# Kernel tuning notes

Measured on AMD Instinct MI355X. Metric: run time of the kernel, lower is better.

## Reference

```python
import jax, jax.numpy as jnp
import numpy as np

SEQ = 2048
D = 2048          # d_model
H = 16            # n_heads
DH = D // H       # dim_per_head = 128 (= pe_rotary_dims, full-head RoPE)
DFF = 4 * D
BACKGROUND_LEN = 1024
STYLE_VECS_LEN = 64


def setup_inputs() -> dict:
    key = jax.random.key(0)
    ks = jax.random.split(key, 12)
    s = 0.02
    f32 = jnp.float32
    return {
        "x": jax.random.normal(ks[0], (SEQ, D), f32),
        "attn_bias": jnp.zeros((SEQ, SEQ), f32),
        "ln_scale": jnp.ones((D,), f32),
        "ln_offset": jnp.zeros((D,), f32),
        "Wq": (jax.random.normal(ks[1], (D, D), f32) * s),
        "Wk": (jax.random.normal(ks[2], (D, D), f32) * s),
        "Wv": (jax.random.normal(ks[3], (D, D), f32) * s),
        "Wo": (jax.random.normal(ks[4], (D, D), f32) * s),
        "W1": (jax.random.normal(ks[5], (D, DFF), f32) * s),
        "b1": jnp.zeros((DFF,), f32),
        "W2": (jax.random.normal(ks[6], (DFF, D), f32) * s),
        "b2": jnp.zeros((D,), f32),
    }


def _layernorm(x, scale, offset):
    mean = jnp.mean(x, axis=-1, keepdims=True)
    var = jnp.var(x, axis=-1, keepdims=True)
    return scale * jax.lax.rsqrt(var + 1e-5) * (x - mean) + offset


def _rotate_every_two(x):
    # x: (T, H, d) -> interleaved (-x2, x1)
    x1 = x[:, :, ::2]
    x2 = x[:, :, 1::2]
    return jnp.stack((-x2, x1), axis=-1).reshape(x.shape)


def _apply_rope(q, k):
    rd = q.shape[-1]
    inv_freq = 1.0 / 10000 ** (np.arange(0, rd, 2) / rd)  # (rd/2,)
    pos = jnp.arange(k.shape[0])
    sinusoid = pos[:, None] * inv_freq[None, :]           # (T, rd/2)
    # repeat 'b n -> b (n j)', j=2  ==  elementwise repeat along last axis
    sin = jnp.repeat(jnp.sin(sinusoid), 2, axis=-1)[:, None, :]  # (T,1,rd)
    cos = jnp.repeat(jnp.cos(sinusoid), 2, axis=-1)[:, None, :]
    q = q * cos + _rotate_every_two(q) * sin
    k = k * cos + _rotate_every_two(k) * sin
    return q, k


def _causal_bottleneck_bias():
    mask = np.tril(np.ones((SEQ, SEQ), np.float32))
    # DO_CAUSAL_BOTTLENECK: tokens after background+style cannot see background
    mask[BACKGROUND_LEN + STYLE_VECS_LEN:, :BACKGROUND_LEN] = 0.0
    return jnp.asarray(-1e10 * (1.0 - mask))


def reference(x, attn_bias, ln_scale, ln_offset, Wq, Wk, Wv, Wo, W1, b1, W2, b2):
    # f_psum / g_psum are identities with cores_per_replica == 1
    xn = _layernorm(x, ln_scale, ln_offset)                      # (T, D)

    q = (xn @ Wq).reshape(SEQ, H, DH)
    k = (xn @ Wk).reshape(SEQ, H, DH)
    v = (xn @ Wv).reshape(SEQ, H, DH)

    q, k = _apply_rope(q, k)  # pe_rotary_dims == dim_per_head: rotate whole head

    logits = jnp.einsum('thd,Thd->htT', q, k) / np.sqrt(DH).astype(x.dtype)
    bias = _causal_bottleneck_bias() + attn_bias                 # (T, T)
    logits = logits + bias[None, :, :]
    weights = jax.nn.softmax(logits, axis=-1)                    # (H, T, T)

    attn_vec = jnp.einsum('htT,Thd->thd', weights, v).reshape(SEQ, D)
    attn_out = attn_vec @ Wo                                     # (T, D)

    ff = jax.nn.gelu(xn @ W1 + b1) @ W2 + b2                     # (T, D)
    return attn_out + ff
```

## Files before the change

### kernel.cpp

```cpp
#include <hip/hip_runtime.h>

#define SEQ 2048
#define DMODEL 2048
#define NH 16
#define DH 128
#define DFF 8192

typedef __bf16 bf16x8 __attribute__((ext_vector_type(8)));
typedef float f32x4 __attribute__((ext_vector_type(4)));
typedef int i32x4 __attribute__((ext_vector_type(4)));

__device__ __forceinline__ float b2f(unsigned short u) {
    union { float f; unsigned int i; } v; v.i = ((unsigned int)u) << 16; return v.f;
}
__device__ __forceinline__ unsigned short f2b(float f) {
    union { float f; unsigned int i; } v; v.f = f;
    unsigned int i = v.i;
    i += 0x7fffu + ((i >> 16) & 1u);
    return (unsigned short)(i >> 16);
}
__device__ __forceinline__ bf16x8 ldfrag(const unsigned short* p) {
    return *(const bf16x8*)p;
}
__device__ __forceinline__ void async_ld16(const unsigned short* g, unsigned short* l) {
    __builtin_amdgcn_global_load_lds(
        (const __attribute__((address_space(1))) unsigned int*)g,
        (__attribute__((address_space(3))) unsigned int*)l, 16, 0, 0);
}
__device__ __forceinline__ float loadef(const void* p, long i, int isf) {
    return isf ? ((const float*)p)[i] : b2f(((const unsigned short*)p)[i]);
}
__device__ __forceinline__ void load8f(const void* p, long i, int isf, float* v) {
    if (isf) {
        i32x4 r0 = *(const i32x4*)((const float*)p + i);
        i32x4 r1 = *(const i32x4*)((const float*)p + i + 4);
        const float* f0 = (const float*)&r0;
        const float* f1 = (const float*)&r1;
#pragma unroll
        for (int j = 0; j < 4; j++) { v[j] = f0[j]; v[4 + j] = f1[j]; }
    } else {
        i32x4 raw = *(const i32x4*)((const unsigned short*)p + i);
        const unsigned short* u = (const unsigned short*)&raw;
#pragma unroll
        for (int j = 0; j < 8; j++) v[j] = b2f(u[j]);
    }
}

__global__ __launch_bounds__(256) void detect_kernel(const unsigned short* __restrict__ x,
                                                     int* __restrict__ flag)
{
    const int tid = threadIdx.x;
    int bad = 0;
#pragma unroll
    for (int i = 0; i < 16; i++) {
        unsigned short u = x[tid * 16 + i];
        int e = (u >> 7) & 0xFF;
        if (e >= 0x90) bad = 1;
    }
    unsigned long long b = __ballot(bad);
    __shared__ int r[4];
    if ((tid & 63) == 0) r[tid >> 6] = (b != 0ull);
    __syncthreads();
    if (tid == 0) *flag = (r[0] | r[1] | r[2] | r[3]) ? 1 : 0;
}

__global__ __launch_bounds__(256) void ln_kernel(
    const void* __restrict__ x,
    const void* __restrict__ sc,
    const void* __restrict__ of,
    unsigned short* __restrict__ xn,
    const int* __restrict__ fl)
{
    const int isf = *fl;
    const int row = blockIdx.x, tid = threadIdx.x;
    float v[8]; float s = 0.f, sq = 0.f;
    load8f(x, (long)row * DMODEL + tid * 8, isf, v);
#pragma unroll
    for (int i = 0; i < 8; i++) { s += v[i]; sq += v[i] * v[i]; }
#pragma unroll
    for (int off = 1; off < 64; off <<= 1) { s += __shfl_xor(s, off); sq += __shfl_xor(sq, off); }
    __shared__ float red[8];
    const int w = tid >> 6, l = tid & 63;
    if (l == 0) { red[w * 2] = s; red[w * 2 + 1] = sq; }
    __syncthreads();
    s  = red[0] + red[2] + red[4] + red[6];
    sq = red[1] + red[3] + red[5] + red[7];
    const float mean = s * (1.0f / DMODEL);
    const float var  = sq * (1.0f / DMODEL) - mean * mean;
    const float rsig = rsqrtf(var + 1e-5f);
    __align__(16) unsigned short o[8];
#pragma unroll
    for (int i = 0; i < 8; i++) {
        int c = tid * 8 + i;
        o[i] = f2b(loadef(sc, c, isf) * (v[i] - mean) * rsig + loadef(of, c, isf));
    }
    *(i32x4*)(xn + (long)row * DMODEL + tid * 8) = *(const i32x4*)o;
}

__global__ __launch_bounds__(1024) void transpose_w(
    const void* __restrict__ in, unsigned short* __restrict__ out, int R, int C,
    const int* __restrict__ fl)
{
    const int isf = *fl;
    __shared__ unsigned short tile[32][33];
    const int tx = threadIdx.x, ty = threadIdx.y;
    const int c0 = blockIdx.x * 32, r0 = blockIdx.y * 32;
    tile[ty][tx] = f2b(loadef(in, (long)(r0 + ty) * C + c0 + tx, isf));
    __syncthreads();
    out[(long)(c0 + ty) * R + r0 + tx] = tile[tx][ty];
}

__global__ __launch_bounds__(256) void rope_kernel(unsigned short* q, unsigned short* k)
{
    const int idx = blockIdx.x * 256 + threadIdx.x;
    const int i = idx & 63;
    const int h = (idx >> 6) & 15;
    const int t = idx >> 10;
    const long base = (long)t * DMODEL + h * DH + 2 * i;
    const float inv = __expf(-(float)i * (9.210340371976184f / 64.0f));
    float sn, cs;
    sincosf((float)t * inv, &sn, &cs);
    {
        float a = b2f(q[base]), b = b2f(q[base + 1]);
        q[base]     = f2b(a * cs - b * sn);
        q[base + 1] = f2b(b * cs + a * sn);
    }
    {
        float a = b2f(k[base]), b = b2f(k[base + 1]);
        k[base]     = f2b(a * cs - b * sn);
        k[base + 1] = f2b(b * cs + a * sn);
    }
}

template<int EPI>
__global__ __launch_bounds__(256) void gemm_bt(
    const unsigned short* __restrict__ A,
    const unsigned short* __restrict__ Bt,
    const void* __restrict__ bias,
    const unsigned short* __restrict__ add,
    void* __restrict__ Cout,
    int M, int N, int K, int Ks,
    const int* __restrict__ fl)
{
    const int isf = fl ? *fl : 0;
    __shared__ __align__(16) unsigned short lA[128 * 32];
    __shared__ __align__(16) unsigned short lB[128 * 32];
    const int tid = threadIdx.x;
    const int l = tid & 63, w = tid >> 6;
    const int quad = l >> 4, lq = l & 15;
    const long bm = (long)blockIdx.y * 128, bn = (long)blockIdx.x * 128;
    const int wm = (w >> 1) * 64, wn = (w & 1) * 64;
    const int kofs = (EPI == 5) ? blockIdx.z * Ks : 0;

    const int srow = w * 32 + (l >> 2);
    const int scol = (l & 3) * 8;
    const unsigned short* Ag0 = A  + (bm + srow) * (long)K + kofs + scol;
    const unsigned short* Ag1 = Ag0 + 16 * (long)K;
    const unsigned short* Bg0 = Bt + (bn + srow) * (long)K + kofs + scol;
    const unsigned short* Bg1 = Bg0 + 16 * (long)K;
    unsigned short* lAd = lA + w * 1024 + l * 8;
    unsigned short* lBd = lB + w * 1024 + l * 8;

    f32x4 acc[4][4] = {};

    for (int k0 = 0; k0 < Ks; k0 += 32) {
        async_ld16(Ag0 + k0, lAd);
        async_ld16(Ag1 + k0, lAd + 512);
        async_ld16(Bg0 + k0, lBd);
        async_ld16(Bg1 + k0, lBd + 512);
        __syncthreads();
        bf16x8 af[4], bfv[4];
#pragma unroll
        for (int i = 0; i < 4; i++) af[i]  = ldfrag(lA + (wm + i * 16 + lq) * 32 + quad * 8);
#pragma unroll
        for (int j = 0; j < 4; j++) bfv[j] = ldfrag(lB + (wn + j * 16 + lq) * 32 + quad * 8);
#pragma unroll
        for (int i = 0; i < 4; i++)
#pragma unroll
            for (int j = 0; j < 4; j++)
                acc[i][j] = __builtin_amdgcn_mfma_f32_16x16x32_bf16(af[i], bfv[j], acc[i][j], 0, 0, 0);
        __syncthreads();
    }

#pragma unroll
    for (int i = 0; i < 4; i++)
#pragma unroll
        for (int j = 0; j < 4; j++)
#pragma unroll
            for (int r = 0; r < 4; r++) {
                const long t = bm + wm + i * 16 + quad * 4 + r;
                const long n = bn + wn + j * 16 + lq;
                float v = acc[i][j][r];
                if constexpr (EPI == 5) {
                    ((float*)Cout)[(long)blockIdx.z * M * N + t * N + n] = v;
                } else if constexpr (EPI == 4) {
                    unsigned short* base = (unsigned short*)Cout;
                    if (n < 4096)
                        base[(n >> 11) * (long)(SEQ * DMODEL) + t * DMODEL + (n & 2047)] = f2b(v);
                    else {
                        const long np = n - 4096;
                        base[2L * SEQ * DMODEL + (np >> 7) * (long)(DH * SEQ) + (np & 127) * (long)SEQ + t] = f2b(v);
                    }
                } else if constexpr (EPI == 3) {
                    v += loadef(bias, n, isf) + b2f(add[t * (long)N + n]);
                    if (isf) ((float*)Cout)[t * (long)N + n] = v;
                    else     ((unsigned short*)Cout)[t * (long)N + n] = f2b(v);
                } else {
                    if constexpr (EPI == 2) {
                        v += loadef(bias, n, isf);
                        v = 0.5f * v * (1.0f + tanhf(0.7978845608028654f * (v + 0.044715f * v * v * v)));
                    }
                    ((unsigned short*)Cout)[t * (long)N + n] = f2b(v);
                }
            }
}

__global__ __launch_bounds__(256) void reduce_out(
    const float* __restrict__ P, int nsplit,
    const unsigned short* __restrict__ aout,
    const void* __restrict__ b2,
    void* __restrict__ out,
    const int* __restrict__ fl)
{
    const int isf = *fl;
    const long i = ((long)blockIdx.x * 256 + threadIdx.x) * 4;
    f32x4 s = *(const f32x4*)(P + i);
    for (int z = 1; z < nsplit; z++) s += *(const f32x4*)(P + (long)z * SEQ * DMODEL + i);
    const unsigned short* a4 = aout + i;
    float v[4];
#pragma unroll
    for (int c = 0; c < 4; c++)
        v[c] = s[c] + b2f(a4[c]) + loadef(b2, (i + c) & (DMODEL - 1), isf);
    if (isf) {
        f32x4 o; o[0] = v[0]; o[1] = v[1]; o[2] = v[2]; o[3] = v[3];
        *(f32x4*)((float*)out + i) = o;
    } else {
        __align__(8) unsigned short o[4];
#pragma unroll
        for (int c = 0; c < 4; c++) o[c] = f2b(v[c]);
        *(unsigned long long*)((unsigned short*)out + i) = *(const unsigned long long*)o;
    }
}

__global__ __launch_bounds__(256) void flash_attn(
    const unsigned short* __restrict__ q,
    const unsigned short* __restrict__ k,
    const unsigned short* __restrict__ vT,
    const void* __restrict__ bias,
    unsigned short* __restrict__ outp,
    const int* __restrict__ fl)
{
    const int isf = *fl;
    __shared__ __align__(16) unsigned short lK[64 * 136];
    __shared__ __align__(16) unsigned short lV[128 * 72];
    __shared__ __align__(16) unsigned short lP[4 * 16 * 72];
    const int tid = threadIdx.x;
    const int l = tid & 63, w = tid >> 6;
    const int quad = l >> 4, lq = l & 15;
    const int qb = blockIdx.x * 64;
    const int h = blockIdx.y;

    bf16x8 aq[4];
#pragma unroll
    for (int c = 0; c < 4; c++)
        aq[c] = ldfrag(q + (long)(qb + 16 * w + lq) * DMODEL + h * DH + 32 * c + quad * 8);

    f32x4 accO[8] = {};
    float m_i[4], l_i[4];
#pragma unroll
    for (int r = 0; r < 4; r++) { m_i[r] = -1e30f; l_i[r] = 0.f; }

    const int Tstart = (qb >= 1088) ? 1024 : 0;
    unsigned short* lPw = lP + w * (16 * 72);

    for (int Tt = Tstart; Tt < qb + 64; Tt += 64) {
        __syncthreads();
#pragma unroll
        for (int s = 0; s < 4; s++) {
            const int cc = tid + 256 * s;
            const int rr = cc >> 4, d0 = (cc & 15) * 8;
            *(i32x4*)(lK + rr * 136 + d0) =
                *(const i32x4*)(k + (long)(Tt + rr) * DMODEL + h * DH + d0);
            const int dd = cc >> 3, t0 = (cc & 7) * 8;
            *(i32x4*)(lV + dd * 72 + t0) =
                *(const i32x4*)(vT + (long)h * (DH * SEQ) + (long)dd * SEQ + Tt + t0);
        }
        __syncthreads();

        float sv[4][4];
        float mx[4] = { -1e30f, -1e30f, -1e30f, -1e30f };
#pragma unroll
        for (int j = 0; j < 4; j++) {
            f32x4 accS = {};
#pragma unroll
            for (int c = 0; c < 4; c++) {
                bf16x8 bk = ldfrag(lK + (j * 16 + lq) * 136 + 32 * c + quad * 8);
                accS = __builtin_amdgcn_mfma_f32_16x16x32_bf16(aq[c], bk, accS, 0, 0, 0);
            }
            const int Tcol = Tt + j * 16 + lq;
#pragma unroll
            for (int r = 0; r < 4; r++) {
                const int trow = qb + 16 * w + quad * 4 + r;
                float s;
                if (Tcol > trow) s = -1e30f;
                else s = accS[r] * 0.08838834764831845f + loadef(bias, (long)trow * SEQ + Tcol, isf);
                sv[j][r] = s;
                mx[r] = fmaxf(mx[r], s);
            }
        }
#pragma unroll
        for (int r = 0; r < 4; r++) {
            mx[r] = fmaxf(mx[r], __shfl_xor(mx[r], 1));
            mx[r] = fmaxf(mx[r], __shfl_xor(mx[r], 2));
            mx[r] = fmaxf(mx[r], __shfl_xor(mx[r], 4));
            mx[r] = fmaxf(mx[r], __shfl_xor(mx[r], 8));
        }
        float alpha[4];
#pragma unroll
        for (int r = 0; r < 4; r++) {
            const float mn = fmaxf(m_i[r], mx[r]);
            alpha[r] = __expf(m_i[r] - mn);
            m_i[r] = mn;
            float sum = 0.f;
#pragma unroll
            for (int j = 0; j < 4; j++) {
                const float p = __expf(sv[j][r] - mn);
                sv[j][r] = p;
                sum += p;
            }
            sum += __shfl_xor(sum, 1);
            sum += __shfl_xor(sum, 2);
            sum += __shfl_xor(sum, 4);
            sum += __shfl_xor(sum, 8);
            l_i[r] = l_i[r] * alpha[r] + sum;
        }
#pragma unroll
        for (int j = 0; j < 4; j++)
#pragma unroll
            for (int r = 0; r < 4; r++)
                lPw[(quad * 4 + r) * 72 + j * 16 + lq] = f2b(sv[j][r]);
#pragma unroll
        for (int jd = 0; jd < 8; jd++)
#pragma unroll
            for (int r = 0; r < 4; r++)
                accO[jd][r] *= alpha[r];
        const bf16x8 ap0 = ldfrag(lPw + lq * 72 + quad * 8);
        const bf16x8 ap1 = ldfrag(lPw + lq * 72 + 32 + quad * 8);
#pragma unroll
        for (int jd = 0; jd < 8; jd++) {
            bf16x8 bv0 = ldfrag(lV + (jd * 16 + lq) * 72 + quad * 8);
            accO[jd] = __builtin_amdgcn_mfma_f32_16x16x32_bf16(ap0, bv0, accO[jd], 0, 0, 0);
            bf16x8 bv1 = ldfrag(lV + (jd * 16 + lq) * 72 + 32 + quad * 8);
            accO[jd] = __builtin_amdgcn_mfma_f32_16x16x32_bf16(ap1, bv1, accO[jd], 0, 0, 0);
        }
    }
#pragma unroll
    for (int r = 0; r < 4; r++) {
        const float inv = 1.0f / l_i[r];
        const long trow = qb + 16 * w + quad * 4 + r;
#pragma unroll
        for (int jd = 0; jd < 8; jd++)
            outp[trow * (long)DMODEL + h * DH + jd * 16 + lq] = f2b(accO[jd][r] * inv);
    }
}

extern "C" void kernel_launch(void* const* d_in, const int* in_sizes, int n_in,
                              void* d_out, int out_size, void* d_ws, size_t ws_size,
                              hipStream_t stream)
{
    (void)in_sizes; (void)n_in; (void)out_size;
    const void* x         = d_in[0];
    const void* attn_bias = d_in[1];
    const void* ln_scale  = d_in[2];
    const void* ln_offset = d_in[3];
    const void* Wq = d_in[4];
    const void* Wk = d_in[5];
    const void* Wv = d_in[6];
    const void* Wo = d_in[7];
    const void* W1 = d_in[8];
    const void* b1 = d_in[9];
    const void* W2 = d_in[10];
    const void* b2 = d_in[11];

    char* ws = (char*)d_ws;
    unsigned short* wT   = (unsigned short*)(ws);
    unsigned short* xn   = (unsigned short*)(ws + (32ull << 20));
    unsigned short* qv   = (unsigned short*)(ws + (40ull << 20));
    unsigned short* kv   = (unsigned short*)(ws + (48ull << 20));
    unsigned short* vTb  = (unsigned short*)(ws + (56ull << 20));
    unsigned short* avec = (unsigned short*)(ws + (64ull << 20));
    unsigned short* aout = (unsigned short*)(ws + (72ull << 20));
    unsigned short* hff  = (unsigned short*)(ws + (40ull << 20));
    int* flag            = (int*)(ws + (80ull << 20));
    float* Pf            = (float*)(ws + (81ull << 20));

    int nsplit = 1;
    if (ws_size >= (145ull << 20)) nsplit = 4;
    else if (ws_size >= (113ull << 20)) nsplit = 2;

    const dim3 tb(32, 32);

    detect_kernel<<<1, 256, 0, stream>>>((const unsigned short*)x, flag);

    ln_kernel<<<SEQ, 256, 0, stream>>>(x, ln_scale, ln_offset, xn, flag);

    transpose_w<<<dim3(64, 64), tb, 0, stream>>>(Wq, wT,                   DMODEL, DMODEL, flag);
    transpose_w<<<dim3(64, 64), tb, 0, stream>>>(Wk, wT + 4 * 1024 * 1024, DMODEL, DMODEL, flag);
    transpose_w<<<dim3(64, 64), tb, 0, stream>>>(Wv, wT + 8 * 1024 * 1024, DMODEL, DMODEL, flag);
    gemm_bt<4><<<dim3(48, 16), 256, 0, stream>>>(xn, wT, nullptr, nullptr, qv,
                                                 SEQ, 3 * DMODEL, DMODEL, DMODEL, flag);

    rope_kernel<<<(SEQ * NH * DH / 2) / 256, 256, 0, stream>>>(qv, kv);

    flash_attn<<<dim3(SEQ / 64, NH), 256, 0, stream>>>(qv, kv, vTb, attn_bias, avec, flag);

    transpose_w<<<dim3(64, 64), tb, 0, stream>>>(Wo, wT, DMODEL, DMODEL, flag);
    gemm_bt<0><<<dim3(16, 16), 256, 0, stream>>>(avec, wT, nullptr, nullptr, aout,
                                                 SEQ, DMODEL, DMODEL, DMODEL, flag);

    transpose_w<<<dim3(DFF / 32, DMODEL / 32), tb, 0, stream>>>(W1, wT, DMODEL, DFF, flag);
    gemm_bt<2><<<dim3(DFF / 128, SEQ / 128), 256, 0, stream>>>(xn, wT, b1, nullptr, hff,
                                                               SEQ, DFF, DMODEL, DMODEL, flag);

    transpose_w<<<dim3(DMODEL / 32, DFF / 32), tb, 0, stream>>>(W2, wT, DFF, DMODEL, flag);
    if (nsplit > 1) {
        gemm_bt<5><<<dim3(16, 16, nsplit), 256, 0, stream>>>(hff, wT, nullptr, nullptr, Pf,
                                                             SEQ, DMODEL, DFF, DFF / nsplit, flag);
        reduce_out<<<(SEQ * DMODEL) / (256 * 4), 256, 0, stream>>>(Pf, nsplit, aout, b2, d_out, flag);
    } else {
        gemm_bt<3><<<dim3(16, 16), 256, 0, stream>>>(hff, wT, b2, aout, d_out,
                                                     SEQ, DMODEL, DFF, DFF, flag);
    }
}
```

Measured before the change: 801.6 us.

## Batch weight transposes, widen GEMM K-tile with swizzled LDS, and use a cheaper GELU

The weight transpose kernel now handles two rows per thread, writes packed 32-bit outputs, and takes four weight pointers through blockIdx.z, so Wq/Wk/Wv/Wo are transposed in one launch. The GEMM K-step doubles to 64 and LDS uses an XOR swizzle, which halves the number of barriers per K and is meant to avoid bank conflicts. GELU's tanh is replaced by an exp/rcp form. The larger LDS tiles can reduce occupancy, and the fast-math GELU changes rounding slightly.

```diff
diff --git a/kernel.cpp b/kernel.cpp
--- a/kernel.cpp
+++ b/kernel.cpp
@@ -98,16 +98,23 @@
 }
 
 __global__ __launch_bounds__(1024) void transpose_w(
-    const void* __restrict__ in, unsigned short* __restrict__ out, int R, int C,
+    const void* __restrict__ in0, const void* __restrict__ in1,
+    const void* __restrict__ in2, const void* __restrict__ in3,
+    unsigned short* __restrict__ out, int R, int C,
     const int* __restrict__ fl)
 {
     const int isf = *fl;
-    __shared__ unsigned short tile[32][33];
+    const int z = blockIdx.z;
+    const void* in = (z == 0) ? in0 : (z == 1) ? in1 : (z == 2) ? in2 : in3;
+    unsigned short* dst = out + (long)z * R * C;
+    __shared__ unsigned int tile[32][33];
     const int tx = threadIdx.x, ty = threadIdx.y;
-    const int c0 = blockIdx.x * 32, r0 = blockIdx.y * 32;
-    tile[ty][tx] = f2b(loadef(in, (long)(r0 + ty) * C + c0 + tx, isf));
+    const int c0 = blockIdx.x * 32, r0 = blockIdx.y * 64;
+    const float a0 = loadef(in, (long)(r0 + 2 * ty)     * C + c0 + tx, isf);
+    const float a1 = loadef(in, (long)(r0 + 2 * ty + 1) * C + c0 + tx, isf);
+    tile[ty][tx] = (unsigned)f2b(a0) | ((unsigned)f2b(a1) << 16);
     __syncthreads();
-    out[(long)(c0 + ty) * R + r0 + tx] = tile[tx][ty];
+    *(unsigned int*)(dst + (long)(c0 + ty) * R + r0 + 2 * tx) = tile[tx][ty];
 }
 
 __global__ __launch_bounds__(256) void rope_kernel(unsigned short* q, unsigned short* k)
@@ -143,8 +150,8 @@
     const int* __restrict__ fl)
 {
     const int isf = fl ? *fl : 0;
-    __shared__ __align__(16) unsigned short lA[128 * 32];
-    __shared__ __align__(16) unsigned short lB[128 * 32];
+    __shared__ __align__(16) unsigned short lA[128 * 64];
+    __shared__ __align__(16) unsigned short lB[128 * 64];
     const int tid = threadIdx.x;
     const int l = tid & 63, w = tid >> 6;
     const int quad = l >> 4, lq = l & 15;
@@ -152,33 +159,42 @@
     const int wm = (w >> 1) * 64, wn = (w & 1) * 64;
     const int kofs = (EPI == 5) ? blockIdx.z * Ks : 0;
 
-    const int srow = w * 32 + (l >> 2);
-    const int scol = (l & 3) * 8;
-    const unsigned short* Ag0 = A  + (bm + srow) * (long)K + kofs + scol;
-    const unsigned short* Ag1 = Ag0 + 16 * (long)K;
-    const unsigned short* Bg0 = Bt + (bn + srow) * (long)K + kofs + scol;
-    const unsigned short* Bg1 = Bg0 + 16 * (long)K;
-    unsigned short* lAd = lA + w * 1024 + l * 8;
-    unsigned short* lBd = lB + w * 1024 + l * 8;
+    const int r8 = l >> 3;
+    const int csw = ((l & 7) ^ r8) * 8;
+    const unsigned short* Ag = A  + (bm + w * 32 + r8) * (long)K + kofs + csw;
+    const unsigned short* Bg = Bt + (bn + w * 32 + r8) * (long)K + kofs + csw;
+    unsigned short* lAd = lA + w * 2048 + l * 8;
+    unsigned short* lBd = lB + w * 2048 + l * 8;
+    const long K8 = 8 * (long)K;
 
     f32x4 acc[4][4] = {};
 
-    for (int k0 = 0; k0 < Ks; k0 += 32) {
-        async_ld16(Ag0 + k0, lAd);
-        async_ld16(Ag1 + k0, lAd + 512);
-        async_ld16(Bg0 + k0, lBd);
-        async_ld16(Bg1 + k0, lBd + 512);
+    for (int k0 = 0; k0 < Ks; k0 += 64) {
+#pragma unroll
+        for (int q = 0; q < 4; q++) {
+            async_ld16(Ag + k0 + q * K8, lAd + q * 512);
+            async_ld16(Bg + k0 + q * K8, lBd + q * 512);
+        }
         __syncthreads();
-        bf16x8 af[4], bfv[4];
-#pragma unroll
-        for (int i = 0; i < 4; i++) af[i]  = ldfrag(lA + (wm + i * 16 + lq) * 32 + quad * 8);
-#pragma unroll
-        for (int j = 0; j < 4; j++) bfv[j] = ldfrag(lB + (wn + j * 16 + lq) * 32 + quad * 8);
-#pragma unroll
-        for (int i = 0; i < 4; i++)
-#pragma unroll
-            for (int j = 0; j < 4; j++)
-                acc[i][j] = __builtin_amdgcn_mfma_f32_16x16x32_bf16(af[i], bfv[j], acc[i][j], 0, 0, 0);
+#pragma unroll
+        for (int hk = 0; hk < 2; hk++) {
+            bf16x8 af[4], bfv[4];
+#pragma unroll
+            for (int i = 0; i < 4; i++) {
+                const int row = wm + i * 16 + lq;
+                af[i] = ldfrag(lA + row * 64 + ((hk * 4 + quad) ^ (lq & 7)) * 8);
+            }
+#pragma unroll
+            for (int j = 0; j < 4; j++) {
+                const int row = wn + j * 16 + lq;
+                bfv[j] = ldfrag(lB + row * 64 + ((hk * 4 + quad) ^ (lq & 7)) * 8);
+            }
+#pragma unroll
+            for (int i = 0; i < 4; i++)
+#pragma unroll
+                for (int j = 0; j < 4; j++)
+                    acc[i][j] = __builtin_amdgcn_mfma_f32_16x16x32_bf16(af[i], bfv[j], acc[i][j], 0, 0, 0);
+        }
         __syncthreads();
     }
 
@@ -208,7 +224,8 @@
                 } else {
                     if constexpr (EPI == 2) {
                         v += loadef(bias, n, isf);
-                        v = 0.5f * v * (1.0f + tanhf(0.7978845608028654f * (v + 0.044715f * v * v * v)));
+                        const float u = 0.7978845608028654f * (v + 0.044715f * v * v * v);
+                        v = v * (1.0f - __builtin_amdgcn_rcpf(1.0f + __expf(2.0f * u)));
                     }
                     ((unsigned short*)Cout)[t * (long)N + n] = f2b(v);
                 }
@@ -394,6 +411,8 @@
     int* flag            = (int*)(ws + (80ull << 20));
     float* Pf            = (float*)(ws + (81ull << 20));
 
+    (void)vTb; (void)kv;
+
     int nsplit = 1;
     if (ws_size >= (145ull << 20)) nsplit = 4;
     else if (ws_size >= (113ull << 20)) nsplit = 2;
@@ -404,9 +423,8 @@
 
     ln_kernel<<<SEQ, 256, 0, stream>>>(x, ln_scale, ln_offset, xn, flag);
 
-    transpose_w<<<dim3(64, 64), tb, 0, stream>>>(Wq, wT,                   DMODEL, DMODEL, flag);
-    transpose_w<<<dim3(64, 64), tb, 0, stream>>>(Wk, wT + 4 * 1024 * 1024, DMODEL, DMODEL, flag);
-    transpose_w<<<dim3(64, 64), tb, 0, stream>>>(Wv, wT + 8 * 1024 * 1024, DMODEL, DMODEL, flag);
+    transpose_w<<<dim3(64, 32, 4), tb, 0, stream>>>(Wq, Wk, Wv, Wo, wT, DMODEL, DMODEL, flag);
+
     gemm_bt<4><<<dim3(48, 16), 256, 0, stream>>>(xn, wT, nullptr, nullptr, qv,
                                                  SEQ, 3 * DMODEL, DMODEL, DMODEL, flag);
 
@@ -414,15 +432,14 @@
 
     flash_attn<<<dim3(SEQ / 64, NH), 256, 0, stream>>>(qv, kv, vTb, attn_bias, avec, flag);
 
-    transpose_w<<<dim3(64, 64), tb, 0, stream>>>(Wo, wT, DMODEL, DMODEL, flag);
-    gemm_bt<0><<<dim3(16, 16), 256, 0, stream>>>(avec, wT, nullptr, nullptr, aout,
+    gemm_bt<0><<<dim3(16, 16), 256, 0, stream>>>(avec, wT + 12ull * 1024 * 1024, nullptr, nullptr, aout,
                                                  SEQ, DMODEL, DMODEL, DMODEL, flag);
 
-    transpose_w<<<dim3(DFF / 32, DMODEL / 32), tb, 0, stream>>>(W1, wT, DMODEL, DFF, flag);
+    transpose_w<<<dim3(DFF / 32, DMODEL / 64), tb, 0, stream>>>(W1, W1, W1, W1, wT, DMODEL, DFF, flag);
     gemm_bt<2><<<dim3(DFF / 128, SEQ / 128), 256, 0, stream>>>(xn, wT, b1, nullptr, hff,
                                                                SEQ, DFF, DMODEL, DMODEL, flag);
 
-    transpose_w<<<dim3(DMODEL / 32, DFF / 32), tb, 0, stream>>>(W2, wT, DFF, DMODEL, flag);
+    transpose_w<<<dim3(DMODEL / 32, DFF / 64), tb, 0, stream>>>(W2, W2, W2, W2, wT, DFF, DMODEL, flag);
     if (nsplit > 1) {
         gemm_bt<5><<<dim3(16, 16, nsplit), 256, 0, stream>>>(hff, wT, nullptr, nullptr, Pf,
                                                              SEQ, DMODEL, DFF, DFF / nsplit, flag);
```

Result: faster. 699.6 us (-12.7%).
